# Performance work log

Hardware: AMD Instinct MI355X
Metric: run time of the kernel (lower is better)

## Reference

```python
import jax, jax.numpy as jnp
import numpy as np

BIAS = 7  # FP8 E4M3 exponent bias


def _decode(bits):
    # bits [..., 8] in order [s, e3, e2, e1, e0, m2, m1, m0]
    b = bits.astype(jnp.int32)
    s = b[..., 0]
    e = (b[..., 1] << 3) | (b[..., 2] << 2) | (b[..., 3] << 1) | b[..., 4]
    m = (b[..., 5] << 2) | (b[..., 6] << 1) | b[..., 7]
    return s, e, m


def _rne_rshift(M, sh):
    # round-to-nearest-even right shift of non-negative int M by sh (sh >= 0)
    q = M >> sh
    rem = M - (q << sh)
    half = jnp.right_shift(jnp.left_shift(1, sh), 1)  # 2^(sh-1), 0 when sh==0
    up = ((rem > half) | ((rem == half) & ((q & 1) == 1))) & (sh > 0)
    return q + up.astype(jnp.int32)


def setup_inputs() -> dict:
    key = jax.random.key(0)
    ks = jax.random.split(key, 6)
    shape = (1024, 4096)

    def make(k1, k2, k3):
        s = jax.random.randint(k1, shape, 0, 2)
        e = jax.random.randint(k2, shape, 0, 15)  # exclude e=15 (NaN region) for well-defined inputs
        m = jax.random.randint(k3, shape, 0, 8)
        bits = jnp.stack([s, (e >> 3) & 1, (e >> 2) & 1, (e >> 1) & 1, e & 1,
                          (m >> 2) & 1, (m >> 1) & 1, m & 1], axis=-1)
        return bits.astype(jnp.float32)

    return {"a": make(ks[0], ks[1], ks[2]), "b": make(ks[3], ks[4], ks[5])}


def _fp8_mul(a, b):
    sa, ea, ma = _decode(a)
    sb, eb_, mb = _decode(b)
    # significand with implicit bit; subnormals (e==0) use leading-zero-normalized form,
    # identical math to the module's mux_a_leading / shift_calc path
    sig_a = jnp.where(ea == 0, ma, ma + 8)
    sig_b = jnp.where(eb_ == 0, mb, mb + 8)
    exa = jnp.where(ea == 0, 1, ea) - BIAS
    exb = jnp.where(eb_ == 0, 1, eb_) - BIAS
    M = sig_a * sig_b              # exact 8-bit product, <= 225 (the 4x4 array multiplier)
    E = exa + exb - 6              # value = M * 2^E  (each sig in units of 2^-3)
    # MSB position p of M (M in [1, 225] => p in [0, 7])
    p = sum(((M >= (1 << k)).astype(jnp.int32) for k in range(1, 8)), start=jnp.zeros_like(M))
    eb_out = E + p + BIAS          # candidate biased exponent (normalization unit)
    # ---- normal path (eb_out >= 1): RNE round to 3 mantissa bits ----
    sh = p - 3
    shp = jnp.maximum(sh, 0)
    lsh = jnp.maximum(-sh, 0)
    mant4 = jnp.left_shift(_rne_rshift(M, shp), lsh)  # in [8, 16]
    carry = mant4 >> 4                                # rounding overflow -> exp += 1
    mant4 = jnp.where(mant4 == 16, 8, mant4)
    e_n = eb_out + carry
    m_n = mant4 - 8
    nan = e_n >= 16                                   # exponent overflow -> NaN (e=1111, m=111)
    e_n = jnp.where(nan, 15, e_n)
    m_n = jnp.where(nan, 7, m_n)
    # ---- subnormal path (eb_out <= 0): mant = RNE(M * 2^(E+9)), value = mant * 2^-9 ----
    t = E + 9
    mant_s = jnp.left_shift(_rne_rshift(M, jnp.clip(-t, 0, 30)), jnp.maximum(t, 0))
    e_s = jnp.where(mant_s >= 8, 1, 0)                # rounding promoted to smallest normal
    m_s = jnp.where(mant_s >= 8, 0, mant_s)
    # ---- select ----
    is_sub = eb_out <= 0
    e_o = jnp.where(is_sub, e_s, e_n)
    m_o = jnp.where(is_sub, m_s, m_n)
    zero = M == 0                                     # either input true zero
    e_o = jnp.where(zero, 0, e_o)
    m_o = jnp.where(zero, 0, m_o)
    s_o = sa ^ sb
    bits = jnp.stack([s_o, (e_o >> 3) & 1, (e_o >> 2) & 1, (e_o >> 1) & 1, e_o & 1,
                      (m_o >> 2) & 1, (m_o >> 1) & 1, m_o & 1], axis=-1)
    return bits.astype(jnp.float32)


def reference(a, b):
    return _fp8_mul(a, b)
```

## Files before the change

### kernel.cpp

```cpp
#include <hip/hip_runtime.h>


#define BIAS 7
#define KPT 4

typedef float vfloat4 __attribute__((ext_vector_type(4)));

__device__ __forceinline__ int rne_rshift(int M, int sh) {
    int q = M >> sh;
    int rem = M - (q << sh);
    int half = (1 << sh) >> 1;
    int up = ((rem > half) | ((rem == half) & (q & 1))) & (sh > 0);
    return q + up;
}

__device__ __forceinline__ int fp8_mul_byte(int a8, int b8) {
    int sa = a8 >> 7,        sb_ = b8 >> 7;
    int ea = (a8 >> 3) & 15, eb = (b8 >> 3) & 15;
    int ma = a8 & 7,         mb = b8 & 7;

    int sig_a = (ea == 0) ? ma : (ma + 8);
    int sig_b = (eb == 0) ? mb : (mb + 8);
    int exa = ((ea == 0) ? 1 : ea) - BIAS;
    int exb = ((eb == 0) ? 1 : eb) - BIAS;

    int M = sig_a * sig_b;
    int E = exa + exb - 6;

    int p = (M > 0) ? (31 - __clz(M)) : 0;
    int eb_out = E + p + BIAS;

    int sh  = p - 3;
    int shp = (sh > 0) ? sh : 0;
    int lsh = (sh < 0) ? -sh : 0;
    int mant4 = rne_rshift(M, shp) << lsh;
    int carry = mant4 >> 4;
    if (mant4 == 16) mant4 = 8;
    int e_n = eb_out + carry;
    int m_n = mant4 - 8;
    if (e_n >= 16) { e_n = 15; m_n = 7; }

    int t = E + 9;
    int rsh   = (-t < 0) ? 0 : ((-t > 30) ? 30 : -t);
    int lsh_s = (t > 0) ? t : 0;
    int mant_s = rne_rshift(M, rsh) << lsh_s;
    int e_s = (mant_s >= 8) ? 1 : 0;
    int m_s = (mant_s >= 8) ? 0 : mant_s;

    int is_sub = (eb_out <= 0);
    int e_o = is_sub ? e_s : e_n;
    int m_o = is_sub ? m_s : m_n;
    if (M == 0) { e_o = 0; m_o = 0; }
    int s_o = sa ^ sb_;
    return (s_o << 7) | (e_o << 3) | m_o;
}

__device__ __forceinline__ int compact_own(uint4 av, uint4 bv) {
    return (int)(((av.x >> 20) & 8u)   | ((av.y >> 21) & 4u)  |
                 ((av.z >> 22) & 2u)   | ((av.w >> 23) & 1u)  |
                 ((bv.x >> 16) & 128u) | ((bv.y >> 17) & 64u) |
                 ((bv.z >> 18) & 32u)  | ((bv.w >> 19) & 16u));
}

__device__ __forceinline__ void compute_store(int own, int odd, int sbit,
                                              vfloat4* __restrict__ dst) {
    int pp = __builtin_amdgcn_update_dpp(0, own, 0xB1, 0xF, 0xF, true);

    int a8 = odd ? (((pp  & 0xF) << 4)        |  (own & 0xF))
                 : (((own & 0xF) << 4)        |  (pp  & 0xF));
    int b8 = odd ? ((((pp  >> 4) & 0xF) << 4) | ((own >> 4) & 0xF))
                 : ((((own >> 4) & 0xF) << 4) | ((pp  >> 4) & 0xF));

    int r = fp8_mul_byte(a8, b8);

    vfloat4 o;
    o.x = (float)((r >> sbit)       & 1);
    o.y = (float)((r >> (sbit - 1)) & 1);
    o.z = (float)((r >> (sbit - 2)) & 1);
    o.w = (float)((r >> (sbit - 3)) & 1);
    *dst = o;
}

__global__ void __launch_bounds__(256)
fp8_mul_kernel(const uint4* __restrict__ a, const uint4* __restrict__ b,
               vfloat4* __restrict__ out, int n_vec) {
    const int base = blockIdx.x * (256 * KPT) + threadIdx.x;
    const int odd  = threadIdx.x & 1;
    const int sbit = odd ? 3 : 7;

    if (base + 256 * (KPT - 1) < n_vec) {
        uint4 av[KPT], bv[KPT];
#pragma unroll
        for (int k = 0; k < KPT; ++k) {
            av[k] = a[base + 256 * k];
            bv[k] = b[base + 256 * k];
        }
        int own[KPT];
#pragma unroll
        for (int k = 0; k < KPT; ++k) own[k] = compact_own(av[k], bv[k]);
#pragma unroll
        for (int k = 0; k < KPT; ++k)
            compute_store(own[k], odd, sbit, &out[base + 256 * k]);
    } else {
        for (int k = 0; k < KPT; ++k) {
            int j = base + 256 * k;
            if (j >= n_vec) continue;
            uint4 av = a[j];
            uint4 bv = b[j];
            compute_store(compact_own(av, bv), odd, sbit, &out[j]);
        }
    }
}

extern "C" void kernel_launch(void* const* d_in, const int* in_sizes, int n_in,
                              void* d_out, int out_size, void* d_ws, size_t ws_size,
                              hipStream_t stream) {
    const uint4* a = (const uint4*)d_in[0];
    const uint4* b = (const uint4*)d_in[1];
    vfloat4* out = (vfloat4*)d_out;
    int n_vec = in_sizes[0] / 4;
    int block = 256;
    int grid = (n_vec + block * KPT - 1) / (block * KPT);
    fp8_mul_kernel<<<grid, block, 0, stream>>>(a, b, out, n_vec);
}
```

Measured before the change: 306.0 us.

## Switch to grid-stride loop with software-prefetched next iteration loads

Replaces the fixed four-items-per-thread blocking with a persistent grid-stride loop capped at 2048 blocks, loading the next element's inputs before computing and storing the current one. This is meant to overlap memory latency with compute and cut block launch overhead. It also swaps the DPP lane-pair exchange for __shfl_xor, which may be slower (ds_bpermute), and gives fewer independent loads in flight per thread than the previous four-way unroll. The shuffle now happens inside a loop where an early return for out-of-range lanes could leave partners missing, though an even stride keeps pairs aligned.

```diff
diff --git a/kernel.cpp b/kernel.cpp
--- a/kernel.cpp
+++ b/kernel.cpp
@@ -2,7 +2,6 @@
 
 
 #define BIAS 7
-#define KPT 4
 
 typedef float vfloat4 __attribute__((ext_vector_type(4)));
 
@@ -62,9 +61,10 @@
                  ((bv.z >> 18) & 32u)  | ((bv.w >> 19) & 16u));
 }
 
-__device__ __forceinline__ void compute_store(int own, int odd, int sbit,
+__device__ __forceinline__ void compute_store(uint4 av, uint4 bv, int odd, int sbit,
                                               vfloat4* __restrict__ dst) {
-    int pp = __builtin_amdgcn_update_dpp(0, own, 0xB1, 0xF, 0xF, true);
+    int own = compact_own(av, bv);
+    int pp  = __shfl_xor(own, 1);
 
     int a8 = odd ? (((pp  & 0xF) << 4)        |  (own & 0xF))
                  : (((own & 0xF) << 4)        |  (pp  & 0xF));
@@ -83,32 +83,26 @@
 
 __global__ void __launch_bounds__(256)
 fp8_mul_kernel(const uint4* __restrict__ a, const uint4* __restrict__ b,
-               vfloat4* __restrict__ out, int n_vec) {
-    const int base = blockIdx.x * (256 * KPT) + threadIdx.x;
+               vfloat4* __restrict__ out, int n_vec, int stride) {
+    int j = blockIdx.x * blockDim.x + threadIdx.x;
+    if (j >= n_vec) return;
+
     const int odd  = threadIdx.x & 1;
     const int sbit = odd ? 3 : 7;
 
-    if (base + 256 * (KPT - 1) < n_vec) {
-        uint4 av[KPT], bv[KPT];
-#pragma unroll
-        for (int k = 0; k < KPT; ++k) {
-            av[k] = a[base + 256 * k];
-            bv[k] = b[base + 256 * k];
-        }
-        int own[KPT];
-#pragma unroll
-        for (int k = 0; k < KPT; ++k) own[k] = compact_own(av[k], bv[k]);
-#pragma unroll
-        for (int k = 0; k < KPT; ++k)
-            compute_store(own[k], odd, sbit, &out[base + 256 * k]);
-    } else {
-        for (int k = 0; k < KPT; ++k) {
-            int j = base + 256 * k;
-            if (j >= n_vec) continue;
-            uint4 av = a[j];
-            uint4 bv = b[j];
-            compute_store(compact_own(av, bv), odd, sbit, &out[j]);
-        }
+    uint4 av = a[j];
+    uint4 bv = b[j];
+
+    for (;;) {
+        int jn = j + stride;
+        bool more = (jn < n_vec);
+        uint4 av_n, bv_n;
+        if (more) { av_n = a[jn]; bv_n = b[jn]; }
+
+        compute_store(av, bv, odd, sbit, &out[j]);
+
+        if (!more) break;
+        av = av_n; bv = bv_n; j = jn;
     }
 }
 
@@ -120,6 +114,8 @@
     vfloat4* out = (vfloat4*)d_out;
     int n_vec = in_sizes[0] / 4;
     int block = 256;
-    int grid = (n_vec + block * KPT - 1) / (block * KPT);
-    fp8_mul_kernel<<<grid, block, 0, stream>>>(a, b, out, n_vec);
+    int grid_needed = (n_vec + block - 1) / block;
+    int grid = grid_needed < 2048 ? grid_needed : 2048;
+    int stride = grid * block;
+    fp8_mul_kernel<<<grid, block, 0, stream>>>(a, b, out, n_vec, stride);
 }
```

After: 313.8 us. 2.5% more time.
